# Performance work log

Hardware: AMD Instinct MI355X
Metric: run time of the kernel (lower is better)

## Reference

```python
import jax, jax.numpy as jnp
import numpy as np

B = 4096          # batch_size per view
D = 256           # projection feature dim
TEMP_F = 0.5      # temperature_f


def setup_inputs() -> dict:
    key = jax.random.key(0)
    k1, k2 = jax.random.split(key)
    return {
        "h_i": jax.random.normal(k1, (B, D), dtype=jnp.float32),
        "h_j": jax.random.normal(k2, (B, D), dtype=jnp.float32),
    }


def reference(h_i, h_j):
    # NT-Xent contrastive loss (forward_feature).
    batch = h_i.shape[0]
    N = 2 * batch
    h = jnp.concatenate([h_i, h_j], axis=0)                 # [N, D]
    sim = (h @ h.T) / TEMP_F                                # [N, N]

    # positives: sim(i, i+batch) and sim(i+batch, i)
    sim_i_j = jnp.diagonal(sim, offset=batch)               # [batch]
    sim_j_i = jnp.diagonal(sim, offset=-batch)              # [batch]
    pos = jnp.concatenate([sim_i_j, sim_j_i], axis=0)       # [N]

    # Torch builds logits = [pos_i, negatives_i] per row where negatives are
    # sim[i, :] with the diagonal AND the positive-pair entry removed, then
    # takes CE with label 0. Since the removed positive-pair entry equals
    # pos_i itself, logsumexp(logits_i) == logsumexp(sim[i, :] with only the
    # diagonal masked). So: loss_i = logsumexp(sim_masked[i]) - pos_i.
    neg_inf = jnp.finfo(sim.dtype).min
    eye = jnp.eye(N, dtype=bool)
    sim_masked = jnp.where(eye, neg_inf, sim)               # mask self-similarity
    lse = jax.nn.logsumexp(sim_masked, axis=1)              # [N]

    # CrossEntropyLoss(reduction='sum') / N  == mean over rows
    loss = jnp.mean(lse - pos)
    return loss
```

## Files before the change

kernel.cpp:

```cpp
#include <hip/hip_runtime.h>
#include <hip/hip_bf16.h>
#include <stdint.h>

#define BATCH 4096
#define N_TOT 8192
#define D_DIM 256
#define SHIFT 150.0f
#define SQRT2 1.41421356237309515f

typedef __bf16 bf16_t;
typedef bf16_t bf16x8 __attribute__((ext_vector_type(8)));
typedef bf16_t bf16x4 __attribute__((ext_vector_type(4)));
typedef float f32x4 __attribute__((ext_vector_type(4)));

__device__ __forceinline__ void gl_lds16(const void* g, void* l) {
  __builtin_amdgcn_global_load_lds(
      (const __attribute__((address_space(1))) void*)(uintptr_t)g,
      (__attribute__((address_space(3))) void*)(uint32_t)(uintptr_t)l,
      16, 0, 0);
}

__global__ void k_prep(const float* __restrict__ hi, const float* __restrict__ hj,
                       bf16_t* __restrict__ hb, float* __restrict__ Zrow,
                       float* __restrict__ posPartial) {
  const int wave = threadIdx.x >> 6, lane = threadIdx.x & 63;
  const int r = blockIdx.x * 4 + wave;
  const size_t off = (size_t)r * D_DIM + lane * 4;
  float4 a = *(const float4*)(hi + off);
  float4 b = *(const float4*)(hj + off);

  bf16x4 oa, ob;
  oa[0] = (bf16_t)(a.x * SQRT2); oa[1] = (bf16_t)(a.y * SQRT2);
  oa[2] = (bf16_t)(a.z * SQRT2); oa[3] = (bf16_t)(a.w * SQRT2);
  ob[0] = (bf16_t)(b.x * SQRT2); ob[1] = (bf16_t)(b.y * SQRT2);
  ob[2] = (bf16_t)(b.z * SQRT2); ob[3] = (bf16_t)(b.w * SQRT2);
  *(bf16x4*)(hb + off) = oa;
  *(bf16x4*)(hb + (size_t)BATCH * D_DIM + off) = ob;

  float d = a.x * b.x + a.y * b.y + a.z * b.z + a.w * b.w;
#pragma unroll
  for (int o = 32; o >= 1; o >>= 1) d += __shfl_xor(d, o);
  __shared__ float ps[4];
  if (lane == 0) ps[wave] = d;
  if (threadIdx.x < 8) Zrow[blockIdx.x * 8 + threadIdx.x] = 0.f;
  __syncthreads();
  if (threadIdx.x == 0) posPartial[blockIdx.x] = ps[0] + ps[1] + ps[2] + ps[3];
}

__global__ __launch_bounds__(512, 6) void k_gemm(const bf16_t* __restrict__ hb,
                                                 float* __restrict__ Zrow) {
  const int t = blockIdx.x;
  int bj = (int)((sqrtf(8.0f * (float)t + 1.0f) - 1.0f) * 0.5f);
  while ((bj + 1) * (bj + 2) / 2 <= t) ++bj;
  while (bj * (bj + 1) / 2 > t) --bj;
  const int bi = t - bj * (bj + 1) / 2;
  const int rBase = bi * 128;
  const int cBase = bj * 128;
  const bool diag = (bi == bj);

  __shared__ __align__(16) bf16_t As[128][64];
  __shared__ __align__(16) bf16_t Bs[128][64];
  const int tid = threadIdx.x;
  const int lane = tid & 63;
  const int wave = tid >> 6;

  const size_t stageRow = (size_t)((wave < 4 ? rBase : cBase) + (wave & 3) * 32);
  const int c_src = (lane & 7) ^ (lane >> 3);
  const bf16_t* gsrc = hb + stageRow * D_DIM + (size_t)(lane >> 3) * D_DIM + c_src * 8;
  bf16_t* lbase = (wave < 4) ? &As[(wave & 3) * 32][0] : &Bs[(wave & 3) * 32][0];

  const int wm = wave >> 1, wn = wave & 1;
  const int quad = lane >> 4, l16 = lane & 15;
  const int sw = l16 & 7;

  f32x4 acc[2][4];
#pragma unroll
  for (int i = 0; i < 2; ++i)
#pragma unroll
    for (int j = 0; j < 4; ++j) acc[i][j] = (f32x4){0.f, 0.f, 0.f, 0.f};

#pragma unroll
  for (int kc = 0; kc < 4; ++kc) {
    __syncthreads();
#pragma unroll
    for (int i = 0; i < 4; ++i)
      gl_lds16(gsrc + (size_t)i * 8 * D_DIM + kc * 64, lbase + i * 8 * 64);
    __syncthreads();
#pragma unroll
    for (int ks = 0; ks < 2; ++ks) {
      bf16x8 af[2], bfr[4];
      const int chunk = ((ks * 4 + quad) ^ sw) * 8;
#pragma unroll
      for (int mt = 0; mt < 2; ++mt)
        af[mt] = *(const bf16x8*)&As[wm * 32 + mt * 16 + l16][chunk];
#pragma unroll
      for (int nt = 0; nt < 4; ++nt)
        bfr[nt] = *(const bf16x8*)&Bs[wn * 64 + nt * 16 + l16][chunk];
#pragma unroll
      for (int mt = 0; mt < 2; ++mt)
#pragma unroll
        for (int nt = 0; nt < 4; ++nt)
          acc[mt][nt] = __builtin_amdgcn_mfma_f32_16x16x32_bf16(af[mt], bfr[nt],
                                                                acc[mt][nt], 0, 0, 0);
    }
  }

  const int rW = rBase + wm * 32 + quad * 4;
  const int cW = cBase + wn * 64 + l16;
  float colAcc[4] = {0.f, 0.f, 0.f, 0.f};
#pragma unroll
  for (int mt = 0; mt < 2; ++mt) {
#pragma unroll
    for (int rg = 0; rg < 4; ++rg) {
      const int rr = rW + mt * 16 + rg;
      float s = 0.f;
#pragma unroll
      for (int nt = 0; nt < 4; ++nt) {
        float e = __expf(acc[mt][nt][rg] - SHIFT);
        if (diag && (rr == cW + nt * 16)) e = 0.f;
        s += e;
        colAcc[nt] += e;
      }
      s += __shfl_xor(s, 1);
      s += __shfl_xor(s, 2);
      s += __shfl_xor(s, 4);
      s += __shfl_xor(s, 8);
      if (l16 == 0) atomicAdd(&Zrow[rr], s);
    }
  }
  if (!diag) {
#pragma unroll
    for (int nt = 0; nt < 4; ++nt) {
      float c = colAcc[nt];
      c += __shfl_xor(c, 16);
      c += __shfl_xor(c, 32);
      if (lane < 16) atomicAdd(&Zrow[cW + nt * 16], c);
    }
  }
}

__global__ void k_finish(const float* __restrict__ Zrow,
                         const float* __restrict__ posPartial,
                         float* __restrict__ out) {
  const int t = threadIdx.x;
  float4 z0 = *(const float4*)(Zrow + t * 8);
  float4 z1 = *(const float4*)(Zrow + t * 8 + 4);
  float sl = __logf(z0.x) + __logf(z0.y) + __logf(z0.z) + __logf(z0.w) +
             __logf(z1.x) + __logf(z1.y) + __logf(z1.z) + __logf(z1.w);
  float sp = posPartial[t];
#pragma unroll
  for (int o = 32; o >= 1; o >>= 1) {
    sl += __shfl_xor(sl, o);
    sp += __shfl_xor(sp, o);
  }
  __shared__ float pl[16], pp[16];
  const int wave = t >> 6, lane = t & 63;
  if (lane == 0) { pl[wave] = sl; pp[wave] = sp; }
  __syncthreads();
  if (t == 0) {
    float L = 0.f, P = 0.f;
    for (int i = 0; i < 16; ++i) { L += pl[i]; P += pp[i]; }
    out[0] = L / (float)N_TOT + SHIFT - P / 2048.0f;
  }
}

extern "C" void kernel_launch(void* const* d_in, const int* in_sizes, int n_in,
                              void* d_out, int out_size, void* d_ws, size_t ws_size,
                              hipStream_t stream) {
  const float* hi = (const float*)d_in[0];
  const float* hj = (const float*)d_in[1];
  float* out = (float*)d_out;

  bf16_t* hb = (bf16_t*)d_ws;
  float* Zrow = (float*)((char*)d_ws + (size_t)N_TOT * D_DIM * 2);
  float* posPartial = Zrow + N_TOT;

  k_prep<<<1024, 256, 0, stream>>>(hi, hj, hb, Zrow, posPartial);
  k_gemm<<<2080, 512, 0, stream>>>(hb, Zrow);
  k_finish<<<1, 1024, 0, stream>>>(Zrow, posPartial, out);
}
```

Baseline: 100.7 us.

## Stage full-K B tile in LDS once and load A fragments directly from global

The k_gemm kernel now copies the whole 128x256 B tile into LDS in one pass with an XOR swizzle, which removes the per-K-chunk barrier pairs. A-operand fragments are read straight from global memory into registers instead of going through LDS. LDS use per block doubles to 64KB and launch bounds drop from 6 to 4 blocks per CU. This trades occupancy and cache-dependent global reads of A for fewer synchronizations.

```diff
diff --git a/kernel.cpp b/kernel.cpp
--- a/kernel.cpp
+++ b/kernel.cpp
@@ -47,7 +47,7 @@
   if (threadIdx.x == 0) posPartial[blockIdx.x] = ps[0] + ps[1] + ps[2] + ps[3];
 }
 
-__global__ __launch_bounds__(512, 6) void k_gemm(const bf16_t* __restrict__ hb,
+__global__ __launch_bounds__(512, 4) void k_gemm(const bf16_t* __restrict__ hb,
                                                  float* __restrict__ Zrow) {
   const int t = blockIdx.x;
   int bj = (int)((sqrtf(8.0f * (float)t + 1.0f) - 1.0f) * 0.5f);
@@ -58,20 +58,30 @@
   const int cBase = bj * 128;
   const bool diag = (bi == bj);
 
-  __shared__ __align__(16) bf16_t As[128][64];
-  __shared__ __align__(16) bf16_t Bs[128][64];
+  __shared__ __align__(16) bf16_t Bs[128][D_DIM];
+
   const int tid = threadIdx.x;
   const int lane = tid & 63;
   const int wave = tid >> 6;
 
-  const size_t stageRow = (size_t)((wave < 4 ? rBase : cBase) + (wave & 3) * 32);
-  const int c_src = (lane & 7) ^ (lane >> 3);
-  const bf16_t* gsrc = hb + stageRow * D_DIM + (size_t)(lane >> 3) * D_DIM + c_src * 8;
-  bf16_t* lbase = (wave < 4) ? &As[(wave & 3) * 32][0] : &Bs[(wave & 3) * 32][0];
+  {
+    const int s = lane >> 5;
+    const int c = lane & 31;
+#pragma unroll
+    for (int i = 0; i < 8; ++i) {
+      const int rloc = wave * 16 + i * 2 + s;
+      const int gc = c ^ (rloc & 15);
+      gl_lds16(hb + (size_t)(cBase + rloc) * D_DIM + gc * 8,
+               &Bs[wave * 16 + i * 2][0]);
+    }
+  }
 
   const int wm = wave >> 1, wn = wave & 1;
   const int quad = lane >> 4, l16 = lane & 15;
-  const int sw = l16 & 7;
+
+  const bf16_t* aBase0 =
+      hb + (size_t)(rBase + wm * 32 + l16) * D_DIM + quad * 8;
+  const bf16_t* aBase1 = aBase0 + (size_t)16 * D_DIM;
 
   f32x4 acc[2][4];
 #pragma unroll
@@ -79,29 +89,23 @@
 #pragma unroll
     for (int j = 0; j < 4; ++j) acc[i][j] = (f32x4){0.f, 0.f, 0.f, 0.f};
 
+  __syncthreads();
+
 #pragma unroll
-  for (int kc = 0; kc < 4; ++kc) {
-    __syncthreads();
+  for (int ks = 0; ks < 8; ++ks) {
+    bf16x8 af0 = *(const bf16x8*)(aBase0 + ks * 32);
+    bf16x8 af1 = *(const bf16x8*)(aBase1 + ks * 32);
+    bf16x8 bfr[4];
+    const int ccol = (((ks * 4 + quad) ^ l16) & 31) * 8;
 #pragma unroll
-    for (int i = 0; i < 4; ++i)
-      gl_lds16(gsrc + (size_t)i * 8 * D_DIM + kc * 64, lbase + i * 8 * 64);
-    __syncthreads();
+    for (int nt = 0; nt < 4; ++nt)
+      bfr[nt] = *(const bf16x8*)&Bs[wn * 64 + nt * 16 + l16][ccol];
 #pragma unroll
-    for (int ks = 0; ks < 2; ++ks) {
-      bf16x8 af[2], bfr[4];
-      const int chunk = ((ks * 4 + quad) ^ sw) * 8;
-#pragma unroll
-      for (int mt = 0; mt < 2; ++mt)
-        af[mt] = *(const bf16x8*)&As[wm * 32 + mt * 16 + l16][chunk];
-#pragma unroll
-      for (int nt = 0; nt < 4; ++nt)
-        bfr[nt] = *(const bf16x8*)&Bs[wn * 64 + nt * 16 + l16][chunk];
-#pragma unroll
-      for (int mt = 0; mt < 2; ++mt)
-#pragma unroll
-        for (int nt = 0; nt < 4; ++nt)
-          acc[mt][nt] = __builtin_amdgcn_mfma_f32_16x16x32_bf16(af[mt], bfr[nt],
-                                                                acc[mt][nt], 0, 0, 0);
+    for (int nt = 0; nt < 4; ++nt) {
+      acc[0][nt] = __builtin_amdgcn_mfma_f32_16x16x32_bf16(af0, bfr[nt],
+                                                           acc[0][nt], 0, 0, 0);
+      acc[1][nt] = __builtin_amdgcn_mfma_f32_16x16x32_bf16(af1, bfr[nt],
+                                                           acc[1][nt], 0, 0, 0);
     }
   }
 
```

New measurement: 117.5 us. 1.17x slower.
